# Kernel optimization log

Measured on AMD Instinct MI355X. Metric: run time of the kernel, lower is better.

The kernel has to match this reference:

```python
import jax, jax.numpy as jnp
import numpy as np

FFT_LEN = 64
BATCH = 262144  # large batch -> memory-bound; per-sample math is a tiny 64x64 DFT
PILOT_IDX = np.array([11, 25, 39, 53])


def _dft_kernels():
    # Exact replication of ComplexIFFT.__init__: cos/sin DFT matrices scaled by 1/N.
    n = np.arange(FFT_LEN).reshape(-1, 1)
    k = np.arange(FFT_LEN)
    cos_k = (np.cos(2.0 * np.pi * k * n / FFT_LEN) / FFT_LEN).astype(np.float32)
    sin_k = (np.sin(2.0 * np.pi * k * n / FFT_LEN) / FFT_LEN).astype(np.float32)
    return jnp.asarray(cos_k), jnp.asarray(sin_k)


def setup_inputs() -> dict:
    key = jax.random.key(0)
    eq_freq = jax.random.normal(key, (BATCH, 2, FFT_LEN), dtype=jnp.float32)
    cos_kernel, sin_kernel = _dft_kernels()
    return {"eq_freq": eq_freq, "cos_kernel": cos_kernel, "sin_kernel": sin_kernel}


def reference(eq_freq, cos_kernel, sin_kernel):
    # insert_pilots: set subcarriers 11/25/39/53 to (1.0 + 0.0j) on every batch row.
    idx = jnp.asarray(PILOT_IDX)
    x = eq_freq.at[:, 0, idx].set(1.0).at[:, 1, idx].set(0.0)  # (B, 2, 64)

    x_real = x[:, 0, :]  # (B, 64)
    x_imag = x[:, 1, :]

    # conv1d(1->64, kernel=64) on a length-64 signal == matmul with the 64x64 kernel:
    # out[b, n] = sum_k kernel[n, k] * x[b, k]
    rr = jnp.einsum('bk,nk->bn', x_real, cos_kernel)
    ri = jnp.einsum('bk,nk->bn', x_imag, cos_kernel)
    ir = jnp.einsum('bk,nk->bn', x_real, sin_kernel)
    ii = jnp.einsum('bk,nk->bn', x_imag, sin_kernel)

    out_real = rr - ii  # (B, 64)
    out_imag = ri + ir

    # torch: permute to (B, 64->len, 1) then cat on dim=1 -> (B, 2, 64) after squeeze semantics;
    # concretely out_real/out_imag each become (B, 1, 64) and are concatenated on dim 1.
    return jnp.stack([out_real, out_imag], axis=1)  # (B, 2, 64)
```

## Files before the change

kernel.cpp:

```cpp
#include <hip/hip_runtime.h>

typedef __attribute__((ext_vector_type(8))) short short8;
typedef __attribute__((ext_vector_type(4))) float float4v;

static __device__ inline short f2bf(float f) {
    union { float f; unsigned u; } v; v.f = f;
    unsigned u = v.u;
    u += 0x7fffu + ((u >> 16) & 1u);
    return (short)(u >> 16);
}

__global__ __launch_bounds__(256)
void build_wt(const float* __restrict__ cosk, const float* __restrict__ sink,
              short* __restrict__ wt)
{
    const int idx = blockIdx.x * 256 + threadIdx.x;
    const int n = idx >> 7, k = idx & 127;
    const int nn = n & 63, km = k & 63;
    float v;
    if (n < 64) v = (k < 64) ? cosk[n * 64 + k] : -sink[n * 64 + km];
    else        v = (k < 64) ? sink[nn * 64 + k] : cosk[nn * 64 + km];
    wt[idx] = f2bf(v);
}

__global__ __launch_bounds__(256, 2)
void ofdm_idft_kernel(const float* __restrict__ eq,
                      const short* __restrict__ wt,
                      float* __restrict__ out)
{
    const int lane = threadIdx.x & 63;
    const int wave = threadIdx.x >> 6;
    const int m = lane & 15;
    const int q = lane >> 4;
    const int b0 = (blockIdx.x * 4 + wave) * 32;

    const unsigned long long PMASK =
        (1ull << 11) | (1ull << 25) | (1ull << 39) | (1ull << 53);

    float4v x[16];
    const float* a0 = eq + (size_t)(b0 + m) * 128 + q * 8;
    #pragma unroll
    for (int u = 0; u < 2; ++u) {
        const float* a = a0 + u * (16 * 128);
        #pragma unroll
        for (int kk = 0; kk < 4; ++kk) {
            x[u * 8 + kk * 2 + 0] = *(const float4v*)(a + kk * 32);
            x[u * 8 + kk * 2 + 1] = *(const float4v*)(a + kk * 32 + 4);
        }
    }

    short8 xfr[2][4];
    #pragma unroll
    for (int u = 0; u < 2; ++u) {
        #pragma unroll
        for (int kk = 0; kk < 4; ++kk) {
            short8 f;
            #pragma unroll
            for (int j = 0; j < 8; ++j) {
                float xv = (j < 4) ? x[u * 8 + kk * 2][j] : x[u * 8 + kk * 2 + 1][j - 4];
                const int k = kk * 32 + q * 8 + j;
                if ((PMASK >> (k & 63)) & 1ull)
                    xv = (k < 64) ? 1.0f : 0.0f;
                f[j] = f2bf(xv);
            }
            xfr[u][kk] = f;
        }
    }

    float4v acc[2][8];
    #pragma unroll
    for (int u = 0; u < 2; ++u)
        #pragma unroll
        for (int nt = 0; nt < 8; ++nt)
            acc[u][nt] = (float4v){0.f, 0.f, 0.f, 0.f};

    #pragma unroll
    for (int kk = 0; kk < 4; ++kk) {
        short8 wfr[8];
        #pragma unroll
        for (int nt = 0; nt < 8; ++nt)
            wfr[nt] = *(const short8*)(wt + (nt * 16 + m) * 128 + kk * 32 + q * 8);
        #pragma unroll
        for (int nt = 0; nt < 8; ++nt) {
            acc[0][nt] = __builtin_amdgcn_mfma_f32_16x16x32_bf16(
                wfr[nt], xfr[0][kk], acc[0][nt], 0, 0, 0);
            acc[1][nt] = __builtin_amdgcn_mfma_f32_16x16x32_bf16(
                wfr[nt], xfr[1][kk], acc[1][nt], 0, 0, 0);
        }
    }

    #pragma unroll
    for (int u = 0; u < 2; ++u) {
        float* ob = out + (size_t)(b0 + u * 16 + m) * 128 + q * 4;
        #pragma unroll
        for (int nt = 0; nt < 8; ++nt)
            __builtin_nontemporal_store(acc[u][nt], (float4v*)(ob + nt * 16));
    }
}

extern "C" void kernel_launch(void* const* d_in, const int* in_sizes, int n_in,
                              void* d_out, int out_size, void* d_ws, size_t ws_size,
                              hipStream_t stream) {
    const float* eq   = (const float*)d_in[0];
    const float* cosk = (const float*)d_in[1];
    const float* sink = (const float*)d_in[2];
    float* out = (float*)d_out;
    short* wt  = (short*)d_ws;

    hipLaunchKernelGGL(build_wt, dim3(64), dim3(256), 0, stream, cosk, sink, wt);
    hipLaunchKernelGGL(ofdm_idft_kernel, dim3(2048), dim3(256), 0, stream,
                       eq, wt, out);
}
```

Baseline: 268.9 us.

## Loop each wave over four tiles with register prefetch of the next tile

The grid shrinks from 2048 to 512 blocks, and each wave now processes four 32-row tiles strided by 2048 tile indices. Loads for the next tile are issued into registers right after the current tile is converted to bf16, so global load latency can overlap with the MFMA work and stores. Output stores also switch from nontemporal to ordinary stores. The trade-off is fewer resident waves to hide latency and extra register pressure from the prefetch buffer.

```diff
diff --git a/kernel.cpp b/kernel.cpp
--- a/kernel.cpp
+++ b/kernel.cpp
@@ -32,70 +32,86 @@
     const int wave = threadIdx.x >> 6;
     const int m = lane & 15;
     const int q = lane >> 4;
-    const int b0 = (blockIdx.x * 4 + wave) * 32;
+    const int wg = blockIdx.x * 4 + wave;
 
     const unsigned long long PMASK =
         (1ull << 11) | (1ull << 25) | (1ull << 39) | (1ull << 53);
 
-    float4v x[16];
-    const float* a0 = eq + (size_t)(b0 + m) * 128 + q * 8;
+#define ISSUE_TILE(TILE)                                                     \
+    {                                                                        \
+        const float* a0 = eq + (size_t)((TILE) * 32 + m) * 128 + q * 8;      \
+        _Pragma("unroll")                                                    \
+        for (int u = 0; u < 2; ++u) {                                        \
+            const float* a = a0 + u * (16 * 128);                            \
+            _Pragma("unroll")                                                \
+            for (int kk = 0; kk < 4; ++kk) {                                 \
+                xb[u * 8 + kk * 2 + 0] = *(const float4v*)(a + kk * 32);     \
+                xb[u * 8 + kk * 2 + 1] = *(const float4v*)(a + kk * 32 + 4); \
+            }                                                                \
+        }                                                                    \
+    }
+
+    float4v xb[16];
+    ISSUE_TILE(wg);
+
     #pragma unroll
-    for (int u = 0; u < 2; ++u) {
-        const float* a = a0 + u * (16 * 128);
+    for (int it = 0; it < 4; ++it) {
+        const int b0 = (wg + it * 2048) * 32;
+
+        short8 xfr[2][4];
+        #pragma unroll
+        for (int u = 0; u < 2; ++u) {
+            #pragma unroll
+            for (int kk = 0; kk < 4; ++kk) {
+                short8 f;
+                #pragma unroll
+                for (int j = 0; j < 8; ++j) {
+                    float xv = (j < 4) ? xb[u * 8 + kk * 2][j]
+                                       : xb[u * 8 + kk * 2 + 1][j - 4];
+                    const int k = kk * 32 + q * 8 + j;
+                    if ((PMASK >> (k & 63)) & 1ull)
+                        xv = (k < 64) ? 1.0f : 0.0f;
+                    f[j] = f2bf(xv);
+                }
+                xfr[u][kk] = f;
+            }
+        }
+
+        if (it < 3) {
+            ISSUE_TILE(wg + (it + 1) * 2048);
+        }
+
+        float4v acc[2][8];
+        #pragma unroll
+        for (int u = 0; u < 2; ++u)
+            #pragma unroll
+            for (int nt = 0; nt < 8; ++nt)
+                acc[u][nt] = (float4v){0.f, 0.f, 0.f, 0.f};
+
         #pragma unroll
         for (int kk = 0; kk < 4; ++kk) {
-            x[u * 8 + kk * 2 + 0] = *(const float4v*)(a + kk * 32);
-            x[u * 8 + kk * 2 + 1] = *(const float4v*)(a + kk * 32 + 4);
+            short8 wfr[8];
+            #pragma unroll
+            for (int nt = 0; nt < 8; ++nt)
+                wfr[nt] = *(const short8*)(wt + (nt * 16 + m) * 128 + kk * 32 + q * 8);
+            #pragma unroll
+            for (int nt = 0; nt < 8; ++nt) {
+                acc[0][nt] = __builtin_amdgcn_mfma_f32_16x16x32_bf16(
+                    wfr[nt], xfr[0][kk], acc[0][nt], 0, 0, 0);
+                acc[1][nt] = __builtin_amdgcn_mfma_f32_16x16x32_bf16(
+                    wfr[nt], xfr[1][kk], acc[1][nt], 0, 0, 0);
+            }
+        }
+
+        #pragma unroll
+        for (int u = 0; u < 2; ++u) {
+            float* ob = out + (size_t)(b0 + u * 16 + m) * 128 + q * 4;
+            #pragma unroll
+            for (int nt = 0; nt < 8; ++nt)
+                *(float4v*)(ob + nt * 16) = acc[u][nt];
         }
     }
-
-    short8 xfr[2][4];
-    #pragma unroll
-    for (int u = 0; u < 2; ++u) {
-        #pragma unroll
-        for (int kk = 0; kk < 4; ++kk) {
-            short8 f;
-            #pragma unroll
-            for (int j = 0; j < 8; ++j) {
-                float xv = (j < 4) ? x[u * 8 + kk * 2][j] : x[u * 8 + kk * 2 + 1][j - 4];
-                const int k = kk * 32 + q * 8 + j;
-                if ((PMASK >> (k & 63)) & 1ull)
-                    xv = (k < 64) ? 1.0f : 0.0f;
-                f[j] = f2bf(xv);
-            }
-            xfr[u][kk] = f;
-        }
-    }
-
-    float4v acc[2][8];
-    #pragma unroll
-    for (int u = 0; u < 2; ++u)
-        #pragma unroll
-        for (int nt = 0; nt < 8; ++nt)
-            acc[u][nt] = (float4v){0.f, 0.f, 0.f, 0.f};
-
-    #pragma unroll
-    for (int kk = 0; kk < 4; ++kk) {
-        short8 wfr[8];
-        #pragma unroll
-        for (int nt = 0; nt < 8; ++nt)
-            wfr[nt] = *(const short8*)(wt + (nt * 16 + m) * 128 + kk * 32 + q * 8);
-        #pragma unroll
-        for (int nt = 0; nt < 8; ++nt) {
-            acc[0][nt] = __builtin_amdgcn_mfma_f32_16x16x32_bf16(
-                wfr[nt], xfr[0][kk], acc[0][nt], 0, 0, 0);
-            acc[1][nt] = __builtin_amdgcn_mfma_f32_16x16x32_bf16(
-                wfr[nt], xfr[1][kk], acc[1][nt], 0, 0, 0);
-        }
-    }
-
-    #pragma unroll
-    for (int u = 0; u < 2; ++u) {
-        float* ob = out + (size_t)(b0 + u * 16 + m) * 128 + q * 4;
-        #pragma unroll
-        for (int nt = 0; nt < 8; ++nt)
-            __builtin_nontemporal_store(acc[u][nt], (float4v*)(ob + nt * 16));
-    }
+#undef ISSUE_TILE
 }
 
 extern "C" void kernel_launch(void* const* d_in, const int* in_sizes, int n_in,
@@ -108,6 +124,6 @@
     short* wt  = (short*)d_ws;
 
     hipLaunchKernelGGL(build_wt, dim3(64), dim3(256), 0, stream, cosk, sink, wt);
-    hipLaunchKernelGGL(ofdm_idft_kernel, dim3(2048), dim3(256), 0, stream,
+    hipLaunchKernelGGL(ofdm_idft_kernel, dim3(512), dim3(256), 0, stream,
                        eq, wt, out);
 }
```

Result: no change. 264.4 us (-1.7%).

## Double-buffer input through LDS with async global_load_lds and coalesced stores

Applied to the files above, without the earlier changes.

Turns the kernel into a persistent loop: each wave handles 8 tiles of 16 rows, prefetching the next tile straight into a double-buffered, XOR-swizzled LDS region with global_load_lds while the current tile is computed. Results are staged back through LDS so each row is written to global memory as contiguous 512-byte chunks instead of strided fragments, and the grid shrinks to 512 blocks using 64KB of dynamic LDS. The aim is to overlap memory latency with compute and improve coalescing on a memory-bound op. In exchange it uses 64KB of LDS per block, which limits occupancy, gives up the nontemporal stores, and depends on correct vmcnt accounting, with no explicit wave barrier between the LDS writes and the reads of other lanes.

```diff
diff --git a/kernel.cpp b/kernel.cpp
--- a/kernel.cpp
+++ b/kernel.cpp
@@ -23,78 +23,100 @@
     wt[idx] = f2bf(v);
 }
 
+typedef __attribute__((address_space(1))) const unsigned g_u32;
+typedef __attribute__((address_space(3))) unsigned l_u32;
+__device__ static inline void gload_lds16(void* l, const void* g) {
+    __builtin_amdgcn_global_load_lds((g_u32*)g, (l_u32*)l, 16, 0, 0);
+}
+
 __global__ __launch_bounds__(256, 2)
 void ofdm_idft_kernel(const float* __restrict__ eq,
                       const short* __restrict__ wt,
                       float* __restrict__ out)
 {
+    extern __shared__ char lds[];
     const int lane = threadIdx.x & 63;
     const int wave = threadIdx.x >> 6;
-    const int m = lane & 15;
-    const int q = lane >> 4;
-    const int b0 = (blockIdx.x * 4 + wave) * 32;
+    const int m    = lane & 15;
+    const int q    = lane >> 4;
+    const int half = lane >> 5;
+    const int pos  = lane & 31;
 
+    char* buf0 = lds + wave * 8192;
+    char* buf1 = lds + 32768 + wave * 8192;
+
+    const int wid = blockIdx.x * 4 + wave;
     const unsigned long long PMASK =
         (1ull << 11) | (1ull << 25) | (1ull << 39) | (1ull << 53);
 
-    float4v x[16];
-    const float* a0 = eq + (size_t)(b0 + m) * 128 + q * 8;
+    auto STAGE = [&](char* B, int it) {
+        const size_t tb = (size_t)(it * 2048 + wid) * 16;
+        #pragma unroll
+        for (int i = 0; i < 8; ++i) {
+            const int r = 2 * i + half;
+            const float* src = eq + (tb + r) * 128 + ((pos ^ (r & 7)) << 2);
+            gload_lds16(B + i * 1024, src);
+        }
+    };
+
+    STAGE(buf0, 0);
+
     #pragma unroll
-    for (int u = 0; u < 2; ++u) {
-        const float* a = a0 + u * (16 * 128);
+    for (int it = 0; it < 8; ++it) {
+        char* cur = (it & 1) ? buf1 : buf0;
+        char* nxt = (it & 1) ? buf0 : buf1;
+        if (it + 1 < 8) STAGE(nxt, it + 1);
+
+        asm volatile("s_waitcnt vmcnt(8)" ::: "memory");
+        __builtin_amdgcn_sched_barrier(0);
+
+        short8 xfr[4];
         #pragma unroll
         for (int kk = 0; kk < 4; ++kk) {
-            x[u * 8 + kk * 2 + 0] = *(const float4v*)(a + kk * 32);
-            x[u * 8 + kk * 2 + 1] = *(const float4v*)(a + kk * 32 + 4);
-        }
-    }
-
-    short8 xfr[2][4];
-    #pragma unroll
-    for (int u = 0; u < 2; ++u) {
-        #pragma unroll
-        for (int kk = 0; kk < 4; ++kk) {
+            const int p0 = kk * 8 + q * 2;
+            float4v lo = *(const float4v*)(cur + m * 512 + ((p0 ^ (m & 7)) << 4));
+            float4v hi = *(const float4v*)(cur + m * 512 + (((p0 + 1) ^ (m & 7)) << 4));
             short8 f;
             #pragma unroll
             for (int j = 0; j < 8; ++j) {
-                float xv = (j < 4) ? x[u * 8 + kk * 2][j] : x[u * 8 + kk * 2 + 1][j - 4];
+                float xv = (j < 4) ? lo[j] : hi[j - 4];
                 const int k = kk * 32 + q * 8 + j;
                 if ((PMASK >> (k & 63)) & 1ull)
                     xv = (k < 64) ? 1.0f : 0.0f;
                 f[j] = f2bf(xv);
             }
-            xfr[u][kk] = f;
+            xfr[kk] = f;
         }
-    }
 
-    float4v acc[2][8];
-    #pragma unroll
-    for (int u = 0; u < 2; ++u)
+        float4v acc[8];
         #pragma unroll
         for (int nt = 0; nt < 8; ++nt)
-            acc[u][nt] = (float4v){0.f, 0.f, 0.f, 0.f};
+            acc[nt] = (float4v){0.f, 0.f, 0.f, 0.f};
+        #pragma unroll
+        for (int kk = 0; kk < 4; ++kk) {
+            short8 wfr[8];
+            #pragma unroll
+            for (int nt = 0; nt < 8; ++nt)
+                wfr[nt] = *(const short8*)(wt + (nt * 16 + m) * 128 + kk * 32 + q * 8);
+            #pragma unroll
+            for (int nt = 0; nt < 8; ++nt)
+                acc[nt] = __builtin_amdgcn_mfma_f32_16x16x32_bf16(
+                    wfr[nt], xfr[kk], acc[nt], 0, 0, 0);
+        }
 
-    #pragma unroll
-    for (int kk = 0; kk < 4; ++kk) {
-        short8 wfr[8];
-        #pragma unroll
-        for (int nt = 0; nt < 8; ++nt)
-            wfr[nt] = *(const short8*)(wt + (nt * 16 + m) * 128 + kk * 32 + q * 8);
         #pragma unroll
         for (int nt = 0; nt < 8; ++nt) {
-            acc[0][nt] = __builtin_amdgcn_mfma_f32_16x16x32_bf16(
-                wfr[nt], xfr[0][kk], acc[0][nt], 0, 0, 0);
-            acc[1][nt] = __builtin_amdgcn_mfma_f32_16x16x32_bf16(
-                wfr[nt], xfr[1][kk], acc[1][nt], 0, 0, 0);
+            const int p = nt * 4 + q;
+            *(float4v*)(cur + m * 512 + ((p ^ (m & 7)) << 4)) = acc[nt];
         }
-    }
 
-    #pragma unroll
-    for (int u = 0; u < 2; ++u) {
-        float* ob = out + (size_t)(b0 + u * 16 + m) * 128 + q * 4;
+        const size_t ob = (size_t)(it * 2048 + wid) * 16 * 128;
         #pragma unroll
-        for (int nt = 0; nt < 8; ++nt)
-            __builtin_nontemporal_store(acc[u][nt], (float4v*)(ob + nt * 16));
+        for (int i = 0; i < 8; ++i) {
+            const int r = 2 * i + half;
+            float4v vv = *(const float4v*)(cur + r * 512 + ((pos ^ (r & 7)) << 4));
+            *(float4v*)(out + ob + r * 128 + pos * 4) = vv;
+        }
     }
 }
 
@@ -108,6 +130,6 @@
     short* wt  = (short*)d_ws;
 
     hipLaunchKernelGGL(build_wt, dim3(64), dim3(256), 0, stream, cosk, sink, wt);
-    hipLaunchKernelGGL(ofdm_idft_kernel, dim3(2048), dim3(256), 0, stream,
+    hipLaunchKernelGGL(ofdm_idft_kernel, dim3(512), dim3(256), 65536, stream,
                        eq, wt, out);
 }
```

Measured after the change: 266.5 us. No clear change (-0.9%).
